# Optimization experiments

Measured on AMD Instinct MI355X. Metric: run time of the kernel, lower is better.

The kernel has to match this reference:

```python
import jax, jax.numpy as jnp
import numpy as np

NUM_EMBEDDINGS = 1024
EMBEDDING_DIM = 256
COMMITMENT_COST = 0.25
DECAY = 0.99
EPS = 1e-05
BATCH = 65536


def setup_inputs() -> dict:
    key = jax.random.key(0)
    k1, k2 = jax.random.split(key, 2)
    z_e = jax.random.normal(k1, (BATCH, EMBEDDING_DIM), dtype=jnp.float32)
    embedding = jax.random.normal(k2, (NUM_EMBEDDINGS, EMBEDDING_DIM), dtype=jnp.float32)
    ema_cluster_size = jnp.zeros((NUM_EMBEDDINGS,), dtype=jnp.float32)
    ema_w = embedding  # buffer initialized as a clone of the codebook
    return {"z_e": z_e, "embedding": embedding,
            "ema_cluster_size": ema_cluster_size, "ema_w": ema_w}


def reference(z_e, embedding, ema_cluster_size, ema_w):
    B, D = z_e.shape
    K = embedding.shape[0]

    # Squared L2 distances: ||z||^2 + ||e||^2 - 2 z.e  -> [B, K]
    z_sq = jnp.sum(z_e * z_e, axis=1, keepdims=True)          # [B, 1]
    e_sq = jnp.sum(embedding * embedding, axis=1)[None, :]    # [1, K]
    ze = jnp.matmul(z_e, embedding.T)                         # [B, K]
    distances = z_sq + e_sq - 2.0 * ze

    encoding_indices = jnp.argmin(distances, axis=1)          # [B]

    # Gather instead of one-hot matmul (same math as encodings @ embedding)
    z_q = embedding[encoding_indices]                         # [B, D]
    z_q_st = z_e + jax.lax.stop_gradient(z_q - z_e)

    vq_loss = COMMITMENT_COST * jnp.mean(
        (jax.lax.stop_gradient(z_q) - z_e) ** 2)

    # EMA statistics (training-mode update); segment_sum == one-hot reductions
    cluster_size = jax.ops.segment_sum(
        jnp.ones((B,), dtype=z_e.dtype), encoding_indices, num_segments=K)
    new_ema_cluster_size = DECAY * ema_cluster_size + (1.0 - DECAY) * cluster_size
    dw = jax.ops.segment_sum(z_e, encoding_indices, num_segments=K)  # [K, D]
    new_ema_w = DECAY * ema_w + (1.0 - DECAY) * dw

    n = jnp.sum(new_ema_cluster_size)
    smoothed = (new_ema_cluster_size + EPS) / (n + K * EPS) * n
    new_embedding = new_ema_w / smoothed[:, None]

    avg_probs = cluster_size / B
    perplexity = jnp.exp(-jnp.sum(avg_probs * jnp.log(avg_probs + 1e-10)))

    return (z_q_st, vq_loss, perplexity, encoding_indices,
            new_embedding, new_ema_cluster_size, new_ema_w)
```

## Files before the change

kernel.cpp:

```cpp
#include <hip/hip_runtime.h>
#include <hip/hip_bf16.h>
#include <math.h>

#define BATCH 65536
#define DIM 256
#define KC 1024
#define COMMIT 0.25f
#define DECAY 0.99f
#define EPSV 1e-5f

#define O_ZQ   0
#define O_LOSS 16777216
#define O_PERP 16777217
#define O_IDX  16777218
#define O_EMB  16842754
#define O_NCS  17104898
#define O_NEW  17105922

typedef __attribute__((ext_vector_type(8))) short bf16x8;
typedef __attribute__((ext_vector_type(4))) float f32x4;

typedef __attribute__((address_space(1))) const void* as1_cvp;
typedef __attribute__((address_space(3))) void* as3_vp;

__device__ __forceinline__ void gload_lds16(const void* g, void* l) {
    __builtin_amdgcn_global_load_lds((as1_cvp)g, (as3_vp)l, 16, 0, 0);
}

__device__ __forceinline__ unsigned short bf16_rne(float x) {
    unsigned u = __builtin_bit_cast(unsigned, x);
    unsigned r = (u + 0x7FFFu + ((u >> 16) & 1u)) >> 16;
    return (unsigned short)r;
}
__device__ __forceinline__ float bf16_to_f(unsigned short h) {
    unsigned u = ((unsigned)h) << 16;
    return __builtin_bit_cast(float, u);
}
__device__ __forceinline__ unsigned enc_f32(float f) {
    unsigned u = __builtin_bit_cast(unsigned, f);
    return u ^ ((unsigned)((int)u >> 31) | 0x80000000u);
}

__global__ __launch_bounds__(256) void prep_zero_kernel(
        const float* __restrict__ emb,
        unsigned short* __restrict__ ehi, unsigned short* __restrict__ elo,
        float* __restrict__ e_sq, float* __restrict__ dw,
        int* __restrict__ counts, float* __restrict__ out) {
    int k = blockIdx.x;
    int t = threadIdx.x;
    dw[(size_t)k * DIM + t] = 0.0f;
    if (t == 64) counts[k] = 0;
    if (k == 0 && t == 128) out[O_LOSS] = 0.0f;
    if (t < 64) {
        int lane = t;
        const float4* ep = (const float4*)(emb + (size_t)k * DIM);
        float4 e = ep[lane];
        float x[4] = {e.x, e.y, e.z, e.w};
        unsigned h[4], l[4];
        float s = 0.0f;
        #pragma unroll
        for (int j = 0; j < 4; ++j) {
            h[j] = bf16_rne(x[j]);
            l[j] = bf16_rne(x[j] - bf16_to_f((unsigned short)h[j]));
            s += x[j] * x[j];
        }
        uint2 ph = make_uint2(h[0] | (h[1] << 16), h[2] | (h[3] << 16));
        uint2 pl = make_uint2(l[0] | (l[1] << 16), l[2] | (l[3] << 16));
        int slot = lane >> 1;
        int half = lane & 1;
        int us = k * 256 + ((slot ^ (k & 7)) << 3) + (half << 2);
        *(uint2*)(ehi + us) = ph;
        *(uint2*)(elo + us) = pl;
        for (int off = 32; off; off >>= 1) s += __shfl_down(s, off, 64);
        if (lane == 0) e_sq[k] = s;
    }
}

#define CH_ROWS 16
__global__ __launch_bounds__(256, 2) void argmin_kernel(
        const float* __restrict__ z_e,
        const unsigned short* __restrict__ ehi,
        const unsigned short* __restrict__ elo,
        const float* __restrict__ e_sq,
        unsigned long long* __restrict__ part) {
    __shared__ __align__(16) unsigned short bhi_s[2][CH_ROWS * 256];
    __shared__ __align__(16) unsigned short blo_s[2][CH_ROWS * 256];
    __shared__ float esq_s[512];

    int tid = threadIdx.x;
    int w = tid >> 6;
    int lane = tid & 63;
    int m16 = lane & 15;
    int quad = lane >> 4;
    int half = blockIdx.x & 1;
    int base_m = (blockIdx.x >> 1) * 128 + w * 32;
    const char* ehi_b = (const char*)ehi + half * 262144;
    const char* elo_b = (const char*)elo + half * 262144;

#define STAGE(c, b) { \
    const char* gh_ = ehi_b + (c) * 8192 + tid * 16; \
    const char* gl_ = elo_b + (c) * 8192 + tid * 16; \
    char* lh_ = (char*)(bhi_s[b]) + tid * 16; \
    char* ll_ = (char*)(blo_s[b]) + tid * 16; \
    _Pragma("unroll") for (int r_ = 0; r_ < 2; ++r_) { \
        gload_lds16(gh_ + r_ * 4096, lh_ + r_ * 4096); \
        gload_lds16(gl_ + r_ * 4096, ll_ + r_ * 4096); } }

    STAGE(0, 0)

    esq_s[tid] = e_sq[(half << 9) + tid];
    esq_s[tid + 256] = e_sq[(half << 9) + tid + 256];

    bf16x8 ahi[2][8], alo[2][8];
    #pragma unroll
    for (int f = 0; f < 2; ++f) {
        const float* zr = z_e + (size_t)(base_m + f * 16 + m16) * DIM;
        #pragma unroll
        for (int ks = 0; ks < 8; ++ks) {
            const float4* p = (const float4*)(zr + ks * 32 + quad * 8);
            float4 x0 = p[0], x1 = p[1];
            float xs[8] = {x0.x, x0.y, x0.z, x0.w, x1.x, x1.y, x1.z, x1.w};
            #pragma unroll
            for (int j = 0; j < 8; ++j) {
                unsigned short h = bf16_rne(xs[j]);
                unsigned short l = bf16_rne(xs[j] - bf16_to_f(h));
                ahi[f][ks][j] = (short)h;
                alo[f][ks][j] = (short)l;
            }
        }
    }

    float best0[4] = {1e30f, 1e30f, 1e30f, 1e30f};
    float best1[4] = {1e30f, 1e30f, 1e30f, 1e30f};
    int bk0[4] = {0, 0, 0, 0};
    int bk1[4] = {0, 0, 0, 0};

    const int rsw = (m16 & 7) << 3;

#define COMPUTE(c, b) { \
    f32x4 acc0 = {0.f, 0.f, 0.f, 0.f}; \
    f32x4 acc1 = {0.f, 0.f, 0.f, 0.f}; \
    const unsigned short* bh_row = bhi_s[b] + m16 * 256; \
    const unsigned short* bl_row = blo_s[b] + m16 * 256; \
    _Pragma("unroll") for (int ks_ = 0; ks_ < 8; ++ks_) { \
        int us_off = (((ks_ * 4 + quad) << 3) ^ rsw); \
        bf16x8 bh = *(const bf16x8*)(bh_row + us_off); \
        bf16x8 bl = *(const bf16x8*)(bl_row + us_off); \
        acc0 = __builtin_amdgcn_mfma_f32_16x16x32_bf16(ahi[0][ks_], bh, acc0, 0, 0, 0); \
        acc1 = __builtin_amdgcn_mfma_f32_16x16x32_bf16(ahi[1][ks_], bh, acc1, 0, 0, 0); \
        acc0 = __builtin_amdgcn_mfma_f32_16x16x32_bf16(ahi[0][ks_], bl, acc0, 0, 0, 0); \
        acc1 = __builtin_amdgcn_mfma_f32_16x16x32_bf16(ahi[1][ks_], bl, acc1, 0, 0, 0); \
        acc0 = __builtin_amdgcn_mfma_f32_16x16x32_bf16(alo[0][ks_], bh, acc0, 0, 0, 0); \
        acc1 = __builtin_amdgcn_mfma_f32_16x16x32_bf16(alo[1][ks_], bh, acc1, 0, 0, 0); } \
    int lcol = (c) * 16 + m16; \
    int col = (half << 9) + lcol; \
    float es = esq_s[lcol]; \
    _Pragma("unroll") for (int r_ = 0; r_ < 4; ++r_) { \
        float d0 = es - 2.0f * acc0[r_]; \
        float d1 = es - 2.0f * acc1[r_]; \
        if (d0 < best0[r_]) { best0[r_] = d0; bk0[r_] = col; } \
        if (d1 < best1[r_]) { best1[r_] = d1; bk1[r_] = col; } } }

    __syncthreads();

    for (int c = 0; c < 32; c += 2) {
        STAGE(c + 1, 1)
        COMPUTE(c, 0)
        __syncthreads();
        if (c + 2 < 32) STAGE(c + 2, 0)
        COMPUTE(c + 1, 1)
        __syncthreads();
    }

    #pragma unroll
    for (int off = 1; off < 16; off <<= 1) {
        #pragma unroll
        for (int r = 0; r < 4; ++r) {
            float ov0 = __shfl_xor(best0[r], off, 64);
            int   ok0 = __shfl_xor(bk0[r], off, 64);
            if (ov0 < best0[r] || (ov0 == best0[r] && ok0 < bk0[r])) { best0[r] = ov0; bk0[r] = ok0; }
            float ov1 = __shfl_xor(best1[r], off, 64);
            int   ok1 = __shfl_xor(bk1[r], off, 64);
            if (ov1 < best1[r] || (ov1 == best1[r] && ok1 < bk1[r])) { best1[r] = ov1; bk1[r] = ok1; }
        }
    }
    if (m16 == 0) {
        #pragma unroll
        for (int r = 0; r < 4; ++r) {
            int row0 = base_m + quad * 4 + r;
            int row1 = base_m + 16 + quad * 4 + r;
            unsigned long long k0 =
                ((unsigned long long)enc_f32(best0[r]) << 32) | (unsigned)bk0[r];
            unsigned long long k1 =
                ((unsigned long long)enc_f32(best1[r]) << 32) | (unsigned)bk1[r];
            part[row0 * 2 + half] = k0;
            part[row1 * 2 + half] = k1;
        }
    }
#undef STAGE
#undef COMPUTE
}

__global__ __launch_bounds__(256) void combine_kernel(
        const unsigned long long* __restrict__ part,
        int* __restrict__ idx_out, float* __restrict__ idx_f_out,
        int* __restrict__ counts) {
    __shared__ int h[KC];
    int t = threadIdx.x;
    #pragma unroll
    for (int i = t; i < KC; i += 256) h[i] = 0;
    __syncthreads();
    int base = blockIdx.x * 512;
    #pragma unroll
    for (int j = 0; j < 2; ++j) {
        int row = base + j * 256 + t;
        unsigned long long k0 = part[row * 2];
        unsigned long long k1 = part[row * 2 + 1];
        unsigned long long m = k0 < k1 ? k0 : k1;
        int k = (int)(m & 0xFFFFFFFFu);
        idx_out[row] = k;
        idx_f_out[row] = (float)k;
        atomicAdd(&h[k], 1);
    }
    __syncthreads();
    #pragma unroll
    for (int i = t; i < KC; i += 256) if (h[i]) atomicAdd(&counts[i], h[i]);
}

__global__ __launch_bounds__(1024) void prefix_stats_kernel(
        const int* __restrict__ counts, int* __restrict__ cursor,
        const float* __restrict__ ema_cs, float* __restrict__ out,
        float* __restrict__ n_ws) {
    __shared__ int wsum[16];
    __shared__ float s1[1024];
    __shared__ float s2[1024];
    int t = threadIdx.x;
    int lane = t & 63;
    int wv = t >> 6;
    int c = counts[t];
    int x = c;
    #pragma unroll
    for (int off = 1; off < 64; off <<= 1) {
        int v = __shfl_up(x, off, 64);
        if (lane >= off) x += v;
    }
    if (lane == 63) wsum[wv] = x;
    float cf = (float)c;
    float ncs = DECAY * ema_cs[t] + (1.0f - DECAY) * cf;
    out[O_NCS + t] = ncs;
    float p = cf / (float)BATCH;
    s1[t] = ncs;
    s2[t] = p * logf(p + 1e-10f);
    __syncthreads();
    if (wv == 0) {
        int v = (lane < 16) ? wsum[lane] : 0;
        #pragma unroll
        for (int off = 1; off < 16; off <<= 1) {
            int u = __shfl_up(v, off, 64);
            if (lane >= off) v += u;
        }
        if (lane < 16) wsum[lane] = v;
    }
    __syncthreads();
    int woff = (wv == 0) ? 0 : wsum[wv - 1];
    cursor[t] = woff + x - c;
    for (int s = 512; s; s >>= 1) {
        if (t < s) { s1[t] += s1[t + s]; s2[t] += s2[t + s]; }
        __syncthreads();
    }
    if (t == 0) {
        n_ws[0] = s1[0];
        out[O_PERP] = expf(-s2[0]);
    }
}

__global__ __launch_bounds__(256) void scatter_rows_kernel(
        const int* __restrict__ idx, int* __restrict__ cursor,
        int* __restrict__ sorted_rows) {
    int i = blockIdx.x * 256 + threadIdx.x;
    int k = idx[i];
    int pos = atomicAdd(&cursor[k], 1);
    sorted_rows[pos] = i;
}

#define SEG 64
__global__ __launch_bounds__(256) void dw_zq_kernel(
        const float* __restrict__ z_e, const float* __restrict__ emb,
        const int* __restrict__ idx, const int* __restrict__ sorted_rows,
        float* __restrict__ zq_out, float* __restrict__ dw,
        float* __restrict__ out) {
    __shared__ int rows_s[SEG];
    __shared__ int keys_s[SEG];
    int t = threadIdx.x;
    int w = t >> 6;
    int lane = t & 63;
    int base = blockIdx.x * SEG;
    if (t < SEG) {
        int r = sorted_rows[base + t];
        rows_s[t] = r;
        keys_s[t] = idx[r];
    }
    __syncthreads();

    int c4 = lane * 4;
    float4 acc = make_float4(0.f, 0.f, 0.f, 0.f);
    float lsum = 0.0f;
    int kprev = keys_s[w * 16];
    #pragma unroll
    for (int g = 0; g < 2; ++g) {
        int rowb[8], kb[8];
        float4 zb[8], qb[8];
        #pragma unroll
        for (int u = 0; u < 8; ++u) {
            int i = w * 16 + g * 8 + u;
            rowb[u] = rows_s[i];
            kb[u] = keys_s[i];
        }
        #pragma unroll
        for (int u = 0; u < 8; ++u) {
            zb[u] = *(const float4*)(z_e + (size_t)rowb[u] * DIM + c4);
            qb[u] = *(const float4*)(emb + (size_t)kb[u] * DIM + c4);
        }
        #pragma unroll
        for (int u = 0; u < 8; ++u) {
            float4 z = zb[u], q = qb[u];
            float4 d = make_float4(q.x - z.x, q.y - z.y, q.z - z.z, q.w - z.w);
            float4 o = make_float4(z.x + d.x, z.y + d.y, z.z + d.z, z.w + d.w);
            *(float4*)(zq_out + (size_t)rowb[u] * DIM + c4) = o;
            lsum += d.x * d.x + d.y * d.y + d.z * d.z + d.w * d.w;
            if (kb[u] != kprev) {
                float* dst = dw + (size_t)kprev * DIM + c4;
                atomicAdd(dst + 0, acc.x);
                atomicAdd(dst + 1, acc.y);
                atomicAdd(dst + 2, acc.z);
                atomicAdd(dst + 3, acc.w);
                acc = make_float4(0.f, 0.f, 0.f, 0.f);
                kprev = kb[u];
            }
            acc.x += z.x; acc.y += z.y; acc.z += z.z; acc.w += z.w;
        }
    }
    {
        float* dst = dw + (size_t)kprev * DIM + c4;
        atomicAdd(dst + 0, acc.x);
        atomicAdd(dst + 1, acc.y);
        atomicAdd(dst + 2, acc.z);
        atomicAdd(dst + 3, acc.w);
    }

    __shared__ float red[256];
    red[t] = lsum;
    __syncthreads();
    for (int s = 128; s; s >>= 1) {
        if (t < s) red[t] += red[t + s];
        __syncthreads();
    }
    if (t == 0)
        atomicAdd(out + O_LOSS, red[0] * (COMMIT / ((float)BATCH * (float)DIM)));
}

__global__ __launch_bounds__(256) void finalize_emb(
        const float* __restrict__ ema_w, const float* __restrict__ dw,
        const float* __restrict__ ncs_arr, const float* __restrict__ n_ws,
        float* __restrict__ out_emb, float* __restrict__ out_emaw) {
    int k = blockIdx.x;
    int d = threadIdx.x;
    size_t i = (size_t)k * DIM + d;
    float w = DECAY * ema_w[i] + (1.0f - DECAY) * dw[i];
    out_emaw[i] = w;
    float n = n_ws[0];
    float ncs = ncs_arr[k];
    float smoothed = (ncs + EPSV) / (n + (float)KC * EPSV) * n;
    out_emb[i] = w / smoothed;
}

extern "C" void kernel_launch(void* const* d_in, const int* in_sizes, int n_in,
                              void* d_out, int out_size, void* d_ws, size_t ws_size,
                              hipStream_t stream) {
    const float* z_e    = (const float*)d_in[0];
    const float* emb    = (const float*)d_in[1];
    const float* ema_cs = (const float*)d_in[2];
    const float* ema_w  = (const float*)d_in[3];
    float* out = (float*)d_out;
    float* ws = (float*)d_ws;

    float* dw            = ws;
    unsigned short* ehi  = (unsigned short*)(dw + KC * DIM);
    unsigned short* elo  = ehi + KC * DIM;
    unsigned long long* part = (unsigned long long*)(elo + KC * DIM);
    float* e_sq          = (float*)(part + 2 * BATCH);
    int* idx             = (int*)(e_sq + KC);
    int* counts          = idx + BATCH;
    int* cursor          = counts + KC;
    int* sorted_rows     = cursor + KC;
    float* n_ws          = (float*)(sorted_rows + BATCH);

    prep_zero_kernel<<<dim3(KC), dim3(256), 0, stream>>>(
        emb, ehi, elo, e_sq, dw, counts, out);
    argmin_kernel<<<dim3(BATCH / 128 * 2), dim3(256), 0, stream>>>(
        z_e, ehi, elo, e_sq, part);
    combine_kernel<<<dim3(BATCH / 512), dim3(256), 0, stream>>>(
        part, idx, out + O_IDX, counts);
    prefix_stats_kernel<<<dim3(1), dim3(1024), 0, stream>>>(
        counts, cursor, ema_cs, out, n_ws);
    scatter_rows_kernel<<<dim3(BATCH / 256), dim3(256), 0, stream>>>(
        idx, cursor, sorted_rows);
    dw_zq_kernel<<<dim3(BATCH / SEG), dim3(256), 0, stream>>>(
        z_e, emb, idx, sorted_rows, out + O_ZQ, dw, out);
    finalize_emb<<<dim3(KC), dim3(256), 0, stream>>>(
        ema_w, dw, out + O_NCS, n_ws, out + O_EMB, out + O_NEW);
}
```

Before: 308.3 us.

## Deepen argmin codebook pipeline to 4 LDS stages with 512-thread blocks

```diff
diff --git a/kernel.cpp b/kernel.cpp
--- a/kernel.cpp
+++ b/kernel.cpp
@@ -67,8 +67,8 @@
         uint2 ph = make_uint2(h[0] | (h[1] << 16), h[2] | (h[3] << 16));
         uint2 pl = make_uint2(l[0] | (l[1] << 16), l[2] | (l[3] << 16));
         int slot = lane >> 1;
-        int half = lane & 1;
-        int us = k * 256 + ((slot ^ (k & 7)) << 3) + (half << 2);
+        int half2 = lane & 1;
+        int us = k * 256 + ((slot ^ (k & 7)) << 3) + (half2 << 2);
         *(uint2*)(ehi + us) = ph;
         *(uint2*)(elo + us) = pl;
         for (int off = 32; off; off >>= 1) s += __shfl_down(s, off, 64);
@@ -76,15 +76,15 @@
     }
 }
 
-#define CH_ROWS 16
-__global__ __launch_bounds__(256, 2) void argmin_kernel(
+#define WAITVM(n) asm volatile("s_waitcnt vmcnt(" #n ")" ::: "memory")
+__global__ __launch_bounds__(512, 4) void argmin_kernel(
         const float* __restrict__ z_e,
         const unsigned short* __restrict__ ehi,
         const unsigned short* __restrict__ elo,
         const float* __restrict__ e_sq,
         unsigned long long* __restrict__ part) {
-    __shared__ __align__(16) unsigned short bhi_s[2][CH_ROWS * 256];
-    __shared__ __align__(16) unsigned short blo_s[2][CH_ROWS * 256];
+    __shared__ __align__(16) unsigned short bhi_s[4][16 * 256];
+    __shared__ __align__(16) unsigned short blo_s[4][16 * 256];
     __shared__ float esq_s[512];
 
     int tid = threadIdx.x;
@@ -92,24 +92,19 @@
     int lane = tid & 63;
     int m16 = lane & 15;
     int quad = lane >> 4;
-    int half = blockIdx.x & 1;
-    int base_m = (blockIdx.x >> 1) * 128 + w * 32;
-    const char* ehi_b = (const char*)ehi + half * 262144;
-    const char* elo_b = (const char*)elo + half * 262144;
-
-#define STAGE(c, b) { \
-    const char* gh_ = ehi_b + (c) * 8192 + tid * 16; \
-    const char* gl_ = elo_b + (c) * 8192 + tid * 16; \
-    char* lh_ = (char*)(bhi_s[b]) + tid * 16; \
-    char* ll_ = (char*)(blo_s[b]) + tid * 16; \
-    _Pragma("unroll") for (int r_ = 0; r_ < 2; ++r_) { \
-        gload_lds16(gh_ + r_ * 4096, lh_ + r_ * 4096); \
-        gload_lds16(gl_ + r_ * 4096, ll_ + r_ * 4096); } }
-
-    STAGE(0, 0)
-
-    esq_s[tid] = e_sq[(half << 9) + tid];
-    esq_s[tid + 256] = e_sq[(half << 9) + tid + 256];
+    int hf = blockIdx.x & 1;
+    int base_m = (blockIdx.x >> 1) * 256 + w * 32;
+    const char* ehi_b = (const char*)ehi + hf * 262144;
+    const char* elo_b = (const char*)elo + hf * 262144;
+
+#define STAGE(c) { \
+    int b_ = (c) & 3; \
+    gload_lds16(ehi_b + (c) * 8192 + tid * 16, (char*)(bhi_s[b_]) + tid * 16); \
+    gload_lds16(elo_b + (c) * 8192 + tid * 16, (char*)(blo_s[b_]) + tid * 16); }
+
+    STAGE(0) STAGE(1) STAGE(2) STAGE(3)
+
+    if (tid < 512) esq_s[tid] = e_sq[(hf << 9) + tid];
 
     bf16x8 ahi[2][8], alo[2][8];
     #pragma unroll
@@ -137,11 +132,13 @@
 
     const int rsw = (m16 & 7) << 3;
 
-#define COMPUTE(c, b) { \
+#define COMPUTE(c) { \
+    int b_ = (c) & 3; \
     f32x4 acc0 = {0.f, 0.f, 0.f, 0.f}; \
     f32x4 acc1 = {0.f, 0.f, 0.f, 0.f}; \
-    const unsigned short* bh_row = bhi_s[b] + m16 * 256; \
-    const unsigned short* bl_row = blo_s[b] + m16 * 256; \
+    const unsigned short* bh_row = bhi_s[b_] + m16 * 256; \
+    const unsigned short* bl_row = blo_s[b_] + m16 * 256; \
+    __builtin_amdgcn_s_setprio(1); \
     _Pragma("unroll") for (int ks_ = 0; ks_ < 8; ++ks_) { \
         int us_off = (((ks_ * 4 + quad) << 3) ^ rsw); \
         bf16x8 bh = *(const bf16x8*)(bh_row + us_off); \
@@ -152,8 +149,9 @@
         acc1 = __builtin_amdgcn_mfma_f32_16x16x32_bf16(ahi[1][ks_], bl, acc1, 0, 0, 0); \
         acc0 = __builtin_amdgcn_mfma_f32_16x16x32_bf16(alo[0][ks_], bh, acc0, 0, 0, 0); \
         acc1 = __builtin_amdgcn_mfma_f32_16x16x32_bf16(alo[1][ks_], bh, acc1, 0, 0, 0); } \
+    __builtin_amdgcn_s_setprio(0); \
     int lcol = (c) * 16 + m16; \
-    int col = (half << 9) + lcol; \
+    int col = (hf << 9) + lcol; \
     float es = esq_s[lcol]; \
     _Pragma("unroll") for (int r_ = 0; r_ < 4; ++r_) { \
         float d0 = es - 2.0f * acc0[r_]; \
@@ -161,16 +159,29 @@
         if (d0 < best0[r_]) { best0[r_] = d0; bk0[r_] = col; } \
         if (d1 < best1[r_]) { best1[r_] = d1; bk1[r_] = col; } } }
 
-    __syncthreads();
-
-    for (int c = 0; c < 32; c += 2) {
-        STAGE(c + 1, 1)
-        COMPUTE(c, 0)
-        __syncthreads();
-        if (c + 2 < 32) STAGE(c + 2, 0)
-        COMPUTE(c + 1, 1)
-        __syncthreads();
-    }
+    asm volatile("s_waitcnt vmcnt(6) lgkmcnt(0)" ::: "memory");
+    __builtin_amdgcn_s_barrier();
+
+    for (int c = 0; c < 28; ++c) {
+        COMPUTE(c)
+        __builtin_amdgcn_s_barrier();
+        STAGE(c + 4)
+        WAITVM(6);
+        __builtin_amdgcn_s_barrier();
+    }
+    COMPUTE(28)
+    __builtin_amdgcn_s_barrier();
+    WAITVM(4);
+    __builtin_amdgcn_s_barrier();
+    COMPUTE(29)
+    __builtin_amdgcn_s_barrier();
+    WAITVM(2);
+    __builtin_amdgcn_s_barrier();
+    COMPUTE(30)
+    __builtin_amdgcn_s_barrier();
+    WAITVM(0);
+    __builtin_amdgcn_s_barrier();
+    COMPUTE(31)
 
     #pragma unroll
     for (int off = 1; off < 16; off <<= 1) {
@@ -193,8 +204,8 @@
                 ((unsigned long long)enc_f32(best0[r]) << 32) | (unsigned)bk0[r];
             unsigned long long k1 =
                 ((unsigned long long)enc_f32(best1[r]) << 32) | (unsigned)bk1[r];
-            part[row0 * 2 + half] = k0;
-            part[row1 * 2 + half] = k1;
+            part[row0 * 2 + hf] = k0;
+            part[row1 * 2 + hf] = k1;
         }
     }
 #undef STAGE
@@ -397,7 +408,7 @@
 
     prep_zero_kernel<<<dim3(KC), dim3(256), 0, stream>>>(
         emb, ehi, elo, e_sq, dw, counts, out);
-    argmin_kernel<<<dim3(BATCH / 128 * 2), dim3(256), 0, stream>>>(
+    argmin_kernel<<<dim3(BATCH / 256 * 2), dim3(512), 0, stream>>>(
         z_e, ehi, elo, e_sq, part);
     combine_kernel<<<dim3(BATCH / 512), dim3(256), 0, stream>>>(
         part, idx, out + O_IDX, counts);
```

Result: slower. 616.5 us (+99.9%).

## Compute commitment loss from argmin distances and halve dw_zq segment size

Applied to the files above, without the earlier changes.

```diff
diff --git a/kernel.cpp b/kernel.cpp
--- a/kernel.cpp
+++ b/kernel.cpp
@@ -39,6 +39,10 @@
 __device__ __forceinline__ unsigned enc_f32(float f) {
     unsigned u = __builtin_bit_cast(unsigned, f);
     return u ^ ((unsigned)((int)u >> 31) | 0x80000000u);
+}
+__device__ __forceinline__ float dec_f32(unsigned e) {
+    unsigned u = (e & 0x80000000u) ? (e ^ 0x80000000u) : ~e;
+    return __builtin_bit_cast(float, u);
 }
 
 __global__ __launch_bounds__(256) void prep_zero_kernel(
@@ -67,8 +71,8 @@
         uint2 ph = make_uint2(h[0] | (h[1] << 16), h[2] | (h[3] << 16));
         uint2 pl = make_uint2(l[0] | (l[1] << 16), l[2] | (l[3] << 16));
         int slot = lane >> 1;
-        int half = lane & 1;
-        int us = k * 256 + ((slot ^ (k & 7)) << 3) + (half << 2);
+        int half2 = lane & 1;
+        int us = k * 256 + ((slot ^ (k & 7)) << 3) + (half2 << 2);
         *(uint2*)(ehi + us) = ph;
         *(uint2*)(elo + us) = pl;
         for (int off = 32; off; off >>= 1) s += __shfl_down(s, off, 64);
@@ -82,7 +86,8 @@
         const unsigned short* __restrict__ ehi,
         const unsigned short* __restrict__ elo,
         const float* __restrict__ e_sq,
-        unsigned long long* __restrict__ part) {
+        unsigned long long* __restrict__ part,
+        float* __restrict__ zsq) {
     __shared__ __align__(16) unsigned short bhi_s[2][CH_ROWS * 256];
     __shared__ __align__(16) unsigned short blo_s[2][CH_ROWS * 256];
     __shared__ float esq_s[512];
@@ -92,10 +97,10 @@
     int lane = tid & 63;
     int m16 = lane & 15;
     int quad = lane >> 4;
-    int half = blockIdx.x & 1;
+    int hf = blockIdx.x & 1;
     int base_m = (blockIdx.x >> 1) * 128 + w * 32;
-    const char* ehi_b = (const char*)ehi + half * 262144;
-    const char* elo_b = (const char*)elo + half * 262144;
+    const char* ehi_b = (const char*)ehi + hf * 262144;
+    const char* elo_b = (const char*)elo + hf * 262144;
 
 #define STAGE(c, b) { \
     const char* gh_ = ehi_b + (c) * 8192 + tid * 16; \
@@ -108,10 +113,11 @@
 
     STAGE(0, 0)
 
-    esq_s[tid] = e_sq[(half << 9) + tid];
-    esq_s[tid + 256] = e_sq[(half << 9) + tid + 256];
+    esq_s[tid] = e_sq[(hf << 9) + tid];
+    esq_s[tid + 256] = e_sq[(hf << 9) + tid + 256];
 
     bf16x8 ahi[2][8], alo[2][8];
+    float zs[2] = {0.0f, 0.0f};
     #pragma unroll
     for (int f = 0; f < 2; ++f) {
         const float* zr = z_e + (size_t)(base_m + f * 16 + m16) * DIM;
@@ -126,8 +132,18 @@
                 unsigned short l = bf16_rne(xs[j] - bf16_to_f(h));
                 ahi[f][ks][j] = (short)h;
                 alo[f][ks][j] = (short)l;
+                zs[f] += xs[j] * xs[j];
             }
         }
+    }
+    #pragma unroll
+    for (int f = 0; f < 2; ++f) {
+        zs[f] += __shfl_xor(zs[f], 16, 64);
+        zs[f] += __shfl_xor(zs[f], 32, 64);
+    }
+    if (hf == 0 && quad == 0) {
+        zsq[base_m + m16] = zs[0];
+        zsq[base_m + 16 + m16] = zs[1];
     }
 
     float best0[4] = {1e30f, 1e30f, 1e30f, 1e30f};
@@ -153,7 +169,7 @@
         acc0 = __builtin_amdgcn_mfma_f32_16x16x32_bf16(alo[0][ks_], bh, acc0, 0, 0, 0); \
         acc1 = __builtin_amdgcn_mfma_f32_16x16x32_bf16(alo[1][ks_], bh, acc1, 0, 0, 0); } \
     int lcol = (c) * 16 + m16; \
-    int col = (half << 9) + lcol; \
+    int col = (hf << 9) + lcol; \
     float es = esq_s[lcol]; \
     _Pragma("unroll") for (int r_ = 0; r_ < 4; ++r_) { \
         float d0 = es - 2.0f * acc0[r_]; \
@@ -193,8 +209,8 @@
                 ((unsigned long long)enc_f32(best0[r]) << 32) | (unsigned)bk0[r];
             unsigned long long k1 =
                 ((unsigned long long)enc_f32(best1[r]) << 32) | (unsigned)bk1[r];
-            part[row0 * 2 + half] = k0;
-            part[row1 * 2 + half] = k1;
+            part[row0 * 2 + hf] = k0;
+            part[row1 * 2 + hf] = k1;
         }
     }
 #undef STAGE
@@ -203,14 +219,17 @@
 
 __global__ __launch_bounds__(256) void combine_kernel(
         const unsigned long long* __restrict__ part,
+        const float* __restrict__ zsq,
         int* __restrict__ idx_out, float* __restrict__ idx_f_out,
-        int* __restrict__ counts) {
+        int* __restrict__ counts, float* __restrict__ out) {
     __shared__ int h[KC];
+    __shared__ float red[256];
     int t = threadIdx.x;
     #pragma unroll
     for (int i = t; i < KC; i += 256) h[i] = 0;
     __syncthreads();
     int base = blockIdx.x * 512;
+    float lsum = 0.0f;
     #pragma unroll
     for (int j = 0; j < 2; ++j) {
         int row = base + j * 256 + t;
@@ -221,10 +240,18 @@
         idx_out[row] = k;
         idx_f_out[row] = (float)k;
         atomicAdd(&h[k], 1);
-    }
+        lsum += dec_f32((unsigned)(m >> 32)) + zsq[row];
+    }
+    red[t] = lsum;
     __syncthreads();
     #pragma unroll
     for (int i = t; i < KC; i += 256) if (h[i]) atomicAdd(&counts[i], h[i]);
+    for (int s = 128; s; s >>= 1) {
+        if (t < s) red[t] += red[t + s];
+        __syncthreads();
+    }
+    if (t == 0)
+        atomicAdd(out + O_LOSS, red[0] * (COMMIT / ((float)BATCH * (float)DIM)));
 }
 
 __global__ __launch_bounds__(1024) void prefix_stats_kernel(
@@ -283,12 +310,11 @@
     sorted_rows[pos] = i;
 }
 
-#define SEG 64
+#define SEG 32
 __global__ __launch_bounds__(256) void dw_zq_kernel(
         const float* __restrict__ z_e, const float* __restrict__ emb,
         const int* __restrict__ idx, const int* __restrict__ sorted_rows,
-        float* __restrict__ zq_out, float* __restrict__ dw,
-        float* __restrict__ out) {
+        float* __restrict__ zq_out, float* __restrict__ dw) {
     __shared__ int rows_s[SEG];
     __shared__ int keys_s[SEG];
     int t = threadIdx.x;
@@ -304,41 +330,36 @@
 
     int c4 = lane * 4;
     float4 acc = make_float4(0.f, 0.f, 0.f, 0.f);
-    float lsum = 0.0f;
-    int kprev = keys_s[w * 16];
-    #pragma unroll
-    for (int g = 0; g < 2; ++g) {
-        int rowb[8], kb[8];
-        float4 zb[8], qb[8];
-        #pragma unroll
-        for (int u = 0; u < 8; ++u) {
-            int i = w * 16 + g * 8 + u;
-            rowb[u] = rows_s[i];
-            kb[u] = keys_s[i];
-        }
-        #pragma unroll
-        for (int u = 0; u < 8; ++u) {
-            zb[u] = *(const float4*)(z_e + (size_t)rowb[u] * DIM + c4);
-            qb[u] = *(const float4*)(emb + (size_t)kb[u] * DIM + c4);
-        }
-        #pragma unroll
-        for (int u = 0; u < 8; ++u) {
-            float4 z = zb[u], q = qb[u];
-            float4 d = make_float4(q.x - z.x, q.y - z.y, q.z - z.z, q.w - z.w);
-            float4 o = make_float4(z.x + d.x, z.y + d.y, z.z + d.z, z.w + d.w);
-            *(float4*)(zq_out + (size_t)rowb[u] * DIM + c4) = o;
-            lsum += d.x * d.x + d.y * d.y + d.z * d.z + d.w * d.w;
-            if (kb[u] != kprev) {
-                float* dst = dw + (size_t)kprev * DIM + c4;
-                atomicAdd(dst + 0, acc.x);
-                atomicAdd(dst + 1, acc.y);
-                atomicAdd(dst + 2, acc.z);
-                atomicAdd(dst + 3, acc.w);
-                acc = make_float4(0.f, 0.f, 0.f, 0.f);
-                kprev = kb[u];
-            }
-            acc.x += z.x; acc.y += z.y; acc.z += z.z; acc.w += z.w;
-        }
+    int kprev = keys_s[w * 8];
+    int rowb[8], kb[8];
+    float4 zb[8], qb[8];
+    #pragma unroll
+    for (int u = 0; u < 8; ++u) {
+        int i = w * 8 + u;
+        rowb[u] = rows_s[i];
+        kb[u] = keys_s[i];
+    }
+    #pragma unroll
+    for (int u = 0; u < 8; ++u) {
+        zb[u] = *(const float4*)(z_e + (size_t)rowb[u] * DIM + c4);
+        qb[u] = *(const float4*)(emb + (size_t)kb[u] * DIM + c4);
+    }
+    #pragma unroll
+    for (int u = 0; u < 8; ++u) {
+        float4 z = zb[u], q = qb[u];
+        float4 d = make_float4(q.x - z.x, q.y - z.y, q.z - z.z, q.w - z.w);
+        float4 o = make_float4(z.x + d.x, z.y + d.y, z.z + d.z, z.w + d.w);
+        *(float4*)(zq_out + (size_t)rowb[u] * DIM + c4) = o;
+        if (kb[u] != kprev) {
+            float* dst = dw + (size_t)kprev * DIM + c4;
+            atomicAdd(dst + 0, acc.x);
+            atomicAdd(dst + 1, acc.y);
+            atomicAdd(dst + 2, acc.z);
+            atomicAdd(dst + 3, acc.w);
+            acc = make_float4(0.f, 0.f, 0.f, 0.f);
+            kprev = kb[u];
+        }
+        acc.x += z.x; acc.y += z.y; acc.z += z.z; acc.w += z.w;
     }
     {
         float* dst = dw + (size_t)kprev * DIM + c4;
@@ -347,16 +368,6 @@
         atomicAdd(dst + 2, acc.z);
         atomicAdd(dst + 3, acc.w);
     }
-
-    __shared__ float red[256];
-    red[t] = lsum;
-    __syncthreads();
-    for (int s = 128; s; s >>= 1) {
-        if (t < s) red[t] += red[t + s];
-        __syncthreads();
-    }
-    if (t == 0)
-        atomicAdd(out + O_LOSS, red[0] * (COMMIT / ((float)BATCH * (float)DIM)));
 }
 
 __global__ __launch_bounds__(256) void finalize_emb(
@@ -393,20 +404,21 @@
     int* counts          = idx + BATCH;
     int* cursor          = counts + KC;
     int* sorted_rows     = cursor + KC;
-    float* n_ws          = (float*)(sorted_rows + BATCH);
+    float* zsq           = (float*)(sorted_rows + BATCH);
+    float* n_ws          = zsq + BATCH;
 
     prep_zero_kernel<<<dim3(KC), dim3(256), 0, stream>>>(
         emb, ehi, elo, e_sq, dw, counts, out);
     argmin_kernel<<<dim3(BATCH / 128 * 2), dim3(256), 0, stream>>>(
-        z_e, ehi, elo, e_sq, part);
+        z_e, ehi, elo, e_sq, part, zsq);
     combine_kernel<<<dim3(BATCH / 512), dim3(256), 0, stream>>>(
-        part, idx, out + O_IDX, counts);
+        part, zsq, idx, out + O_IDX, counts, out);
     prefix_stats_kernel<<<dim3(1), dim3(1024), 0, stream>>>(
         counts, cursor, ema_cs, out, n_ws);
     scatter_rows_kernel<<<dim3(BATCH / 256), dim3(256), 0, stream>>>(
         idx, cursor, sorted_rows);
     dw_zq_kernel<<<dim3(BATCH / SEG), dim3(256), 0, stream>>>(
-        z_e, emb, idx, sorted_rows, out + O_ZQ, dw, out);
+        z_e, emb, idx, sorted_rows, out + O_ZQ, dw);
     finalize_emb<<<dim3(KC), dim3(256), 0, stream>>>(
         ema_w, dw, out + O_NCS, n_ws, out + O_EMB, out + O_NEW);
 }
```

Result: slower. 354.0 us (+14.8%).
